# Optimization experiments

Measured on AMD Instinct MI355X. Metric: run time of the kernel, lower is better.

The kernel has to match this reference:

```python
import jax, jax.numpy as jnp
import numpy as np

B, S, D, H, V, L, N, FF = 4, 2048, 768, 4, 32000, 2048, 3, 1024
DH = D // H  # 192; note original scales scores by 1/20, not 1/sqrt(192)


def layernorm(x, g, b):
    m = jnp.mean(x, axis=-1, keepdims=True)
    v = jnp.mean((x - m) ** 2, axis=-1, keepdims=True)
    return (x - m) / jnp.sqrt(v + 1e-5) * g + b


def attn_block(h, Wq, bq, Wk, bk, Wv, bv, g, b, mask):
    Bx, Sx, _ = h.shape
    q = (h @ Wq + bq).reshape(Bx, Sx, H, DH).transpose(0, 2, 1, 3)  # bhsd
    k = (h @ Wk + bk).reshape(Bx, Sx, H, DH).transpose(0, 2, 1, 3)
    v = (h @ Wv + bv).reshape(Bx, Sx, H, DH).transpose(0, 2, 1, 3)
    w = jnp.einsum('bhqd,bhkd->bhqk', q, k) / 20.0
    w = jnp.where(mask, -1e9, w)
    # original code uses Softmax(dim=2), i.e. over the QUERY axis — kept faithful
    a = jax.nn.softmax(w, axis=2)
    o = jnp.einsum('bhqk,bhkd->bhqd', a, v)
    o = o.transpose(0, 2, 1, 3).reshape(Bx, Sx, D)
    return layernorm(h + o, g, b)


def setup_inputs() -> dict:
    key = jax.random.key(0)
    ks = jax.random.split(key, 12)
    sc = 0.02
    n = lambda k, s: jax.random.normal(k, s, jnp.float32) * sc
    return {
        'x': jax.random.randint(ks[0], (B, S), 0, V),
        'label': jax.random.randint(ks[1], (B, S), 0, V),
        'tok_emb': n(ks[2], (V, D)),
        'pos_emb': n(ks[3], (L, D)),
        'Wq': n(ks[4], (N, 2, D, D)), 'bq': jnp.zeros((N, 2, D)),
        'Wk': n(ks[5], (N, 2, D, D)), 'bk': jnp.zeros((N, 2, D)),
        'Wv': n(ks[6], (N, 2, D, D)), 'bv': jnp.zeros((N, 2, D)),
        'ln_g': jnp.ones((N, 2, D)), 'ln_b': jnp.zeros((N, 2, D)),
        'W1': n(ks[7], (N, D, FF)), 'b1': jnp.zeros((N, FF)),
        'W2': n(ks[8], (N, FF, D)), 'b2': jnp.zeros((N, D)),
        'f_g': jnp.ones((N, D)), 'f_b': jnp.zeros((N, D)),
        'Wcls': n(ks[9], (D, V)), 'bcls': jnp.zeros((V,)),
    }


def reference(x, label, tok_emb, pos_emb, Wq, bq, Wk, bk, Wv, bv, ln_g, ln_b,
              W1, b1, W2, b2, f_g, f_b, Wcls, bcls):
    Bx, Sx = x.shape
    pad = (x == 0)[:, None, :, None]                       # [B,1,S,1] masks query rows
    look = jnp.triu(jnp.ones((Sx, Sx), bool), 1)[None, None]
    mask = look | pad                                      # [B,1,S,S] -> broadcast over H
    h = tok_emb[x] + pos_emb[jnp.arange(Sx)][None, :, :]
    for i in range(N):
        for j in range(2):
            h = attn_block(h, Wq[i, j], bq[i, j], Wk[i, j], bk[i, j],
                           Wv[i, j], bv[i, j], ln_g[i, j], ln_b[i, j], mask)
        h1 = jax.nn.relu(h @ W1[i] + b1[i]) @ W2[i] + b2[i]
        h = layernorm(h + h1, f_g[i], f_b[i])
    logits = h @ Wcls + bcls                               # [B,S,V]
    logp = jax.nn.log_softmax(logits, axis=-1)
    loss = -jnp.mean(jnp.take_along_axis(logp, label[..., None], axis=-1))
    return loss
```

## Files before the change

### kernel.cpp

```cpp
#include <hip/hip_runtime.h>
#include <hip/hip_bf16.h>

using u16 = unsigned short;
using u32 = unsigned int;
using bf16x8 = __attribute__((ext_vector_type(8))) short;
using f32x4  = __attribute__((ext_vector_type(4))) float;

namespace {
constexpr int BB   = 4;
constexpr int SEQ  = 2048;
constexpr int DIM  = 768;
constexpr int NH   = 4;
constexpr int DHD  = 192;
constexpr int VOC  = 32000;
constexpr int NLAY = 3;
constexpr int FFD  = 1024;
constexpr int ROWS = BB * SEQ;
constexpr int NT2  = VOC / 256;
constexpr int QKV = 3 * DIM;
constexpr int BH  = BB * NH;
}

__device__ __forceinline__ float b2f(u16 u) { return __uint_as_float(((u32)u) << 16); }
__device__ __forceinline__ u16 f2b(float f) {
    u32 x = __float_as_uint(f);
    return (u16)((x + 0x7fffu + ((x >> 16) & 1u)) >> 16);
}

__device__ __forceinline__ void gload16(const u16* g, u16* l) {
    __builtin_amdgcn_global_load_lds(
        (const __attribute__((address_space(1))) u32*)g,
        (__attribute__((address_space(3))) u32*)l, 16, 0, 0);
}

#define PHASE_END(N) do {                                        \
    __builtin_amdgcn_sched_barrier(0);                           \
    asm volatile("s_waitcnt vmcnt(" #N ")" ::: "memory");        \
    __builtin_amdgcn_s_barrier();                                \
    asm volatile("" ::: "memory");                               \
    __builtin_amdgcn_sched_barrier(0);                           \
} while (0)

__device__ __forceinline__ float block_sum256(float v, float* sb) {
    #pragma unroll
    for (int off = 32; off > 0; off >>= 1) v += __shfl_down(v, off, 64);
    int lane = threadIdx.x & 63, w = threadIdx.x >> 6;
    if (lane == 0) sb[w] = v;
    __syncthreads();
    float r = sb[0] + sb[1] + sb[2] + sb[3];
    __syncthreads();
    return r;
}

template<int MODE>
__global__ __launch_bounds__(512, 2)
void gemm256(const u16* __restrict__ A, long lda,
             const u16* __restrict__ Bt, long ldb,
             int M, int N, int K,
             const float* __restrict__ bias,
             float* __restrict__ Cf, u16* __restrict__ Cb, long ldc,
             int relu,
             int HH, long sAb, long sAh, long sBb, long sBh, long sCb, long sCh,
             const int* __restrict__ xtok, float* __restrict__ cpart,
             const int* __restrict__ label,
             float* __restrict__ partials, float* __restrict__ picked)
{
    __shared__ __align__(16) u16 sA[2][256 * 64];
    __shared__ __align__(16) u16 sB[2][256 * 64];

    int t = threadIdx.x, w = t >> 6, lane = t & 63;
    int wr = w >> 2, wcn = w & 3;
    int lr = lane & 15, lg = lane >> 4, rsw = lr & 7;

    int z = blockIdx.z;
    int bz = z / HH, hz = z % HH;
    const u16* Ab = A + (size_t)bz * sAb + (size_t)hz * sAh;
    const u16* Bb = Bt + (size_t)bz * sBb + (size_t)hz * sBh;
    size_t Coff = (size_t)bz * sCb + (size_t)hz * sCh;

    int bx = blockIdx.x, by = blockIdx.y;
    if (MODE == 1) {
        int tix = blockIdx.x;
        by = 7;
        while (by * (by + 1) / 2 > tix) by--;
        bx = tix - by * (by + 1) / 2;
    } else {
        int pid = by * gridDim.x + bx;
        int xcd = pid & 7, s = pid >> 3;
        bx = s >> 2;
        by = xcd * 4 + (s & 3);
    }
    int m0 = by * 256, n0 = bx * 256;

    int srow = lane >> 3;
    int scol = ((lane & 7) ^ srow) * 8;

    f32x4 acc[8][4];
    #pragma unroll
    for (int i = 0; i < 8; i++)
        #pragma unroll
        for (int j = 0; j < 4; j++) acc[i][j] = (f32x4){0.f, 0.f, 0.f, 0.f};

    auto stageA = [&](int buf, int k0) {
        #pragma unroll
        for (int r = 0; r < 4; r++) {
            int rb = r * 64 + w * 8;
            gload16(Ab + (size_t)(m0 + rb + srow) * lda + k0 + scol,
                    &sA[buf][rb * 64]);
        }
    };
    auto stageB = [&](int buf, int k0, int h) {
        #pragma unroll
        for (int j = 0; j < 2; j++) {
            int rb = (j * 2 + (w >> 2)) * 64 + h * 32 + (w & 3) * 8;
            gload16(Bb + (size_t)(n0 + rb + srow) * ldb + k0 + scol,
                    &sB[buf][rb * 64]);
        }
    };

    {
        int nt = K >> 6;
        stageA(0, 0); stageB(0, 0, 0); stageB(0, 0, 1);
        PHASE_END(0);

        for (int kt = 0; kt < nt; ++kt) {
            int cur = kt & 1;
            int kn = (kt + 1) << 6;
            bool st = (kt + 1 < nt);
            bf16x8 aa[2][8], bb[2][2];
            #pragma unroll
            for (int kx = 0; kx < 2; kx++) {
                int jsw = ((kx * 4 + lg) ^ rsw) * 8;
                #pragma unroll
                for (int mi = 0; mi < 8; mi++)
                    aa[kx][mi] = *(const bf16x8*)&sA[cur][(wr * 128 + mi * 16 + lr) * 64 + jsw];
                #pragma unroll
                for (int ni = 0; ni < 2; ni++)
                    bb[kx][ni] = *(const bf16x8*)&sB[cur][(wcn * 64 + ni * 16 + lr) * 64 + jsw];
            }
            if (st) { stageA(cur ^ 1, kn); stageB(cur ^ 1, kn, 0); }
            __builtin_amdgcn_s_setprio(1);
            #pragma unroll
            for (int kx = 0; kx < 2; kx++)
                #pragma unroll
                for (int mi = 0; mi < 8; mi++)
                    #pragma unroll
                    for (int ni = 0; ni < 2; ni++)
                        acc[mi][ni] = __builtin_amdgcn_mfma_f32_16x16x32_bf16(
                            aa[kx][mi], bb[kx][ni], acc[mi][ni], 0, 0, 0);
            __builtin_amdgcn_s_setprio(0);
            if (st) PHASE_END(6); else PHASE_END(0);
            bf16x8 bc[2][2];
            #pragma unroll
            for (int kx = 0; kx < 2; kx++) {
                int jsw = ((kx * 4 + lg) ^ rsw) * 8;
                #pragma unroll
                for (int ni = 0; ni < 2; ni++)
                    bc[kx][ni] = *(const bf16x8*)&sB[cur][(wcn * 64 + (ni + 2) * 16 + lr) * 64 + jsw];
            }
            if (st) stageB(cur ^ 1, kn, 1);
            __builtin_amdgcn_s_setprio(1);
            #pragma unroll
            for (int kx = 0; kx < 2; kx++)
                #pragma unroll
                for (int mi = 0; mi < 8; mi++)
                    #pragma unroll
                    for (int ni = 0; ni < 2; ni++)
                        acc[mi][ni + 2] = __builtin_amdgcn_mfma_f32_16x16x32_bf16(
                            aa[kx][mi], bc[kx][ni], acc[mi][ni + 2], 0, 0, 0);
            __builtin_amdgcn_s_setprio(0);
            if (st) PHASE_END(2); else PHASE_END(0);
        }
    }

    if (MODE == 1) {
        const int* xb = xtok + (size_t)bz * SEQ;
        float cs[2][4] = {{0.f,0.f,0.f,0.f},{0.f,0.f,0.f,0.f}};
        #pragma unroll
        for (int mi = 0; mi < 8; mi++)
            #pragma unroll
            for (int j = 0; j < 4; j++) {
                int grow = m0 + wr * 128 + mi * 16 + lg * 4 + j;
                int xz = xb[grow];
                #pragma unroll
                for (int ni = 0; ni < 4; ni++) {
                    int gcol = n0 + wcn * 64 + ni * 16 + lr;
                    float v = acc[mi][ni][j] * 0.05f;
                    if (gcol > grow || xz == 0) v = -30.f;
                    float e = __expf(v);
                    Cb[Coff + (size_t)grow * ldc + gcol] = f2b(e);
                    cs[mi >> 2][ni] += e;
                }
            }
        #pragma unroll
        for (int h = 0; h < 2; h++)
            #pragma unroll
            for (int ni = 0; ni < 4; ni++) {
                float c = cs[h][ni];
                c += __shfl_xor(c, 16, 64);
                c += __shfl_xor(c, 32, 64);
                if (lg == 0) {
                    int p = (m0 >> 6) + wr * 2 + h;
                    cpart[((size_t)p * BH + z) * SEQ + n0 + wcn * 64 + ni * 16 + lr] = c;
                }
            }
    } else {
        #pragma unroll
        for (int mi = 0; mi < 8; mi++)
            #pragma unroll
            for (int ni = 0; ni < 4; ni++) {
                int gcol = n0 + wcn * 64 + ni * 16 + lr;
                float bcol = bias[gcol];
                #pragma unroll
                for (int j = 0; j < 4; j++) acc[mi][ni][j] += bcol;
            }
        #pragma unroll
        for (int mi = 0; mi < 8; mi++)
            #pragma unroll
            for (int j = 0; j < 4; j++) {
                int grow = m0 + wr * 128 + mi * 16 + lg * 4 + j;
                int lab = label[grow];
                #pragma unroll
                for (int ni = 0; ni < 4; ni++) {
                    int gcol = n0 + wcn * 64 + ni * 16 + lr;
                    if (lab == gcol) picked[grow] = acc[mi][ni][j];
                }
            }
        float* red = (float*)sA;
        #pragma unroll
        for (int mi = 0; mi < 8; mi++)
            #pragma unroll
            for (int j = 0; j < 4; j++) {
                float mx = -1e30f;
                #pragma unroll
                for (int ni = 0; ni < 4; ni++) mx = fmaxf(mx, acc[mi][ni][j]);
                #pragma unroll
                for (int off = 1; off < 16; off <<= 1)
                    mx = fmaxf(mx, __shfl_xor(mx, off, 64));
                float ss = 0.f;
                #pragma unroll
                for (int ni = 0; ni < 4; ni++) ss += __expf(acc[mi][ni][j] - mx);
                #pragma unroll
                for (int off = 1; off < 16; off <<= 1) ss += __shfl_xor(ss, off, 64);
                if (lr == 0) {
                    int rloc = wr * 128 + mi * 16 + lg * 4 + j;
                    red[rloc * 8 + wcn * 2 + 0] = mx;
                    red[rloc * 8 + wcn * 2 + 1] = ss;
                }
            }
        __syncthreads();
        if (t < 256) {
            float Mv = -1e30f;
            #pragma unroll
            for (int q = 0; q < 4; q++) Mv = fmaxf(Mv, red[t * 8 + q * 2]);
            float Sv = 0.f;
            #pragma unroll
            for (int q = 0; q < 4; q++)
                Sv += red[t * 8 + q * 2 + 1] * __expf(red[t * 8 + q * 2] - Mv);
            size_t row = (size_t)(m0 + t);
            partials[(row * NT2 + bx) * 2 + 0] = Mv;
            partials[(row * NT2 + bx) * 2 + 1] = Sv;
        }
    }
}

template<int MODE>
__global__ __launch_bounds__(256)
void gemm128(const u16* __restrict__ A, long lda,
             const u16* __restrict__ Bt, long ldb,
             int N, int K,
             const float* __restrict__ bias,
             float* __restrict__ Cf, u16* __restrict__ Cb, long ldc, int relu,
             int HH, long sAb, long sAh, long sBb, long sBh, long sCb, long sCh)
{
    __shared__ __align__(16) u16 sA[2][128 * 64];
    __shared__ __align__(16) u16 sB[2][128 * 64];

    int z = blockIdx.z, bz = z / HH, hz = z % HH;
    const u16* Ab = A + (size_t)bz * sAb + (size_t)hz * sAh;
    const u16* Bb = Bt + (size_t)bz * sBb + (size_t)hz * sBh;
    size_t Coff = (size_t)bz * sCb + (size_t)hz * sCh;

    int bx = blockIdx.x, by = blockIdx.y;
    if (MODE == 0 && gridDim.y == 64) {
        int pid = by * gridDim.x + bx;
        int xcd = pid & 7, s = pid >> 3;
        bx = s >> 3;
        by = xcd * 8 + (s & 7);
    }
    if (MODE == 3) {
        by = (by & 1) ? (15 - (by >> 1)) : (by >> 1);
    }
    int m0 = by * 128, n0 = bx * 128;

    int t = threadIdx.x, w = t >> 6, lane = t & 63;
    int wr = w >> 1, wc = w & 1, lr = lane & 15, lg = lane >> 4, rsw = lr & 7;
    int srow = lane >> 3, scol = ((lane & 7) ^ srow) * 8;

    f32x4 acc[4][4];
    #pragma unroll
    for (int i = 0; i < 4; i++)
        #pragma unroll
        for (int j = 0; j < 4; j++) acc[i][j] = (f32x4){0.f, 0.f, 0.f, 0.f};

    auto stageA = [&](int buf, int k0) {
        #pragma unroll
        for (int i = 0; i < 4; i++) {
            int rb = (w * 4 + i) * 8;
            gload16(Ab + (size_t)(m0 + rb + srow) * lda + k0 + scol,
                    &sA[buf][rb * 64]);
        }
    };
    auto stageB = [&](int buf, int k0, int h) {
        #pragma unroll
        for (int j = 0; j < 2; j++) {
            int rb = j * 64 + h * 32 + w * 8;
            int row = n0 + rb + srow;
            if (MODE == 3) { if (row > N - 1) row = N - 1; }
            gload16(Bb + (size_t)row * ldb + k0 + scol, &sB[buf][rb * 64]);
        }
    };

    int nt = K >> 6;
    if (MODE == 3) {
        int ntE = (by + 1) * 2;
        if (ntE < nt) nt = ntE;
    }

    stageA(0, 0); stageB(0, 0, 0); stageB(0, 0, 1);
    PHASE_END(0);

    for (int kt = 0; kt < nt; ++kt) {
        int cur = kt & 1;
        int kn = (kt + 1) << 6;
        bool st = (kt + 1 < nt);
        bf16x8 aa[2][4], bb[2][2];
        #pragma unroll
        for (int kx = 0; kx < 2; kx++) {
            int jsw = ((kx * 4 + lg) ^ rsw) * 8;
            #pragma unroll
            for (int mi = 0; mi < 4; mi++)
                aa[kx][mi] = *(const bf16x8*)&sA[cur][(wr * 64 + mi * 16 + lr) * 64 + jsw];
            #pragma unroll
            for (int ni = 0; ni < 2; ni++)
                bb[kx][ni] = *(const bf16x8*)&sB[cur][(wc * 64 + ni * 16 + lr) * 64 + jsw];
        }
        if (st) { stageA(cur ^ 1, kn); stageB(cur ^ 1, kn, 0); }
        __builtin_amdgcn_s_setprio(1);
        #pragma unroll
        for (int kx = 0; kx < 2; kx++)
            #pragma unroll
            for (int mi = 0; mi < 4; mi++)
                #pragma unroll
                for (int ni = 0; ni < 2; ni++)
                    acc[mi][ni] = __builtin_amdgcn_mfma_f32_16x16x32_bf16(
                        aa[kx][mi], bb[kx][ni], acc[mi][ni], 0, 0, 0);
        __builtin_amdgcn_s_setprio(0);
        if (st) PHASE_END(6); else PHASE_END(0);

        bf16x8 bc[2][2];
        #pragma unroll
        for (int kx = 0; kx < 2; kx++) {
            int jsw = ((kx * 4 + lg) ^ rsw) * 8;
            #pragma unroll
            for (int ni = 0; ni < 2; ni++)
                bc[kx][ni] = *(const bf16x8*)&sB[cur][(wc * 64 + (ni + 2) * 16 + lr) * 64 + jsw];
        }
        if (st) stageB(cur ^ 1, kn, 1);
        __builtin_amdgcn_s_setprio(1);
        #pragma unroll
        for (int kx = 0; kx < 2; kx++)
            #pragma unroll
            for (int mi = 0; mi < 4; mi++)
                #pragma unroll
                for (int ni = 0; ni < 2; ni++)
                    acc[mi][ni + 2] = __builtin_amdgcn_mfma_f32_16x16x32_bf16(
                        aa[kx][mi], bc[kx][ni], acc[mi][ni + 2], 0, 0, 0);
        __builtin_amdgcn_s_setprio(0);
        if (st) PHASE_END(2); else PHASE_END(0);
    }

    #pragma unroll
    for (int mi = 0; mi < 4; mi++)
        #pragma unroll
        for (int ni = 0; ni < 4; ni++)
            #pragma unroll
            for (int j = 0; j < 4; j++) {
                int grow = m0 + wr * 64 + mi * 16 + lg * 4 + j;
                int gcol = n0 + wc * 64 + ni * 16 + lr;
                if (MODE == 3) {
                    if (gcol < N)
                        Cb[Coff + (size_t)grow * ldc + gcol] = f2b(acc[mi][ni][j]);
                } else {
                    float v = acc[mi][ni][j];
                    if (bias) v += bias[gcol];
                    if (relu) v = fmaxf(v, 0.f);
                    size_t ci = Coff + (size_t)grow * ldc + gcol;
                    if (Cf) Cf[ci] = v;
                    if (Cb) Cb[ci] = f2b(v);
                }
            }
}

__global__ __launch_bounds__(256)
void embed_k(const int* __restrict__ x, const float* __restrict__ tok,
             const float* __restrict__ pos, u16* __restrict__ hb)
{
    int row = blockIdx.x, t = threadIdx.x;
    int token = x[row];
    int s = row & (SEQ - 1);
    size_t base = (size_t)row * DIM;
    #pragma unroll
    for (int e = 0; e < 3; e++) {
        int d = t + e * 256;
        float v = tok[(size_t)token * DIM + d] + pos[(size_t)s * DIM + d];
        hb[base + d] = f2b(v);
    }
}

__global__ __launch_bounds__(256)
void resid_ln(const u16* __restrict__ res, const u16* __restrict__ add,
              const float* __restrict__ g, const float* __restrict__ b,
              u16* __restrict__ out)
{
    __shared__ float sb[4];
    int row = blockIdx.x, t = threadIdx.x;
    size_t base = (size_t)row * DIM;
    float x0 = 0.f, x1 = 0.f, x2 = 0.f, x3 = 0.f;
    if (t < 192) {
        ushort4 r4 = *(const ushort4*)&res[base + t * 4];
        ushort4 a4 = *(const ushort4*)&add[base + t * 4];
        x0 = b2f(r4.x) + b2f(a4.x);
        x1 = b2f(r4.y) + b2f(a4.y);
        x2 = b2f(r4.z) + b2f(a4.z);
        x3 = b2f(r4.w) + b2f(a4.w);
    }
    float mean = block_sum256(x0 + x1 + x2 + x3, sb) * (1.f / DIM);
    float d0 = x0 - mean, d1 = x1 - mean, d2 = x2 - mean, d3 = x3 - mean;
    float var = block_sum256(t < 192 ? d0*d0 + d1*d1 + d2*d2 + d3*d3 : 0.f, sb) * (1.f / DIM);
    float rs = rsqrtf(var + 1e-5f);
    if (t < 192) {
        float4 gv = *(const float4*)&g[t * 4];
        float4 bv = *(const float4*)&b[t * 4];
        ushort4 ob = {f2b(d0 * rs * gv.x + bv.x), f2b(d1 * rs * gv.y + bv.y),
                      f2b(d2 * rs * gv.z + bv.z), f2b(d3 * rs * gv.w + bv.w)};
        *(ushort4*)&out[base + t * 4] = ob;
    }
}

__global__ void v_transpose(const u16* __restrict__ v, long ldv,
                            const float* __restrict__ cpart, u16* __restrict__ vT)
{
    __shared__ u16 tile[32][33];
    int z = blockIdx.z;
    int b = z >> 2, h = z & 3;
    int s0 = blockIdx.x * 32, d0 = blockIdx.y * 32;
    int tx = threadIdx.x, ty = threadIdx.y;
    #pragma unroll
    for (int i = 0; i < 4; i++)
        tile[ty + i * 8][tx] = v[((size_t)b * SEQ + s0 + ty + i * 8) * ldv + h * DHD + d0 + tx];
    int scol = s0 + tx;
    int pmin = (scol >> 8) * 4;
    float sv = 0.f;
    for (int p = pmin; p < 32; p++) sv += cpart[((size_t)p * BH + z) * SEQ + scol];
    float inv = 1.f / sv;
    __syncthreads();
    #pragma unroll
    for (int i = 0; i < 4; i++)
        vT[((size_t)z * DHD + d0 + ty + i * 8) * SEQ + scol] =
            f2b(b2f(tile[tx][ty + i * 8]) * inv);
}

__global__ void wt_cvt(const float* __restrict__ src, u16* __restrict__ dst, int K, int N)
{
    __shared__ float tile[32][33];
    int n0 = blockIdx.x * 32, k0 = blockIdx.y * 32;
    int tx = threadIdx.x, ty = threadIdx.y;
    #pragma unroll
    for (int i = 0; i < 4; i++)
        tile[ty + i * 8][tx] = src[(size_t)(k0 + ty + i * 8) * N + n0 + tx];
    __syncthreads();
    #pragma unroll
    for (int i = 0; i < 4; i++)
        dst[(size_t)(n0 + ty + i * 8) * K + k0 + tx] = f2b(tile[tx][ty + i * 8]);
}

__global__ __launch_bounds__(256)
void bias_cat(const float* __restrict__ bq, const float* __restrict__ bk,
              const float* __restrict__ bv, float* __restrict__ dst)
{
    int ij = blockIdx.x, t = threadIdx.x;
    #pragma unroll
    for (int e = 0; e < 3; e++) {
        int d = t + e * 256;
        dst[(size_t)ij * QKV + d]            = bq[(size_t)ij * DIM + d];
        dst[(size_t)ij * QKV + DIM + d]      = bk[(size_t)ij * DIM + d];
        dst[(size_t)ij * QKV + 2 * DIM + d]  = bv[(size_t)ij * DIM + d];
    }
}

__global__ __launch_bounds__(256)
void lse_merge(const float* __restrict__ partials, float* __restrict__ lse)
{
    __shared__ float sm[4], ssum[4];
    int row = blockIdx.x, t = threadIdx.x;
    float m = -1e30f, s = 0.f;
    if (t < NT2) {
        const float* p = partials + ((size_t)row * NT2 + t) * 2;
        m = p[0]; s = p[1];
    }
    #pragma unroll
    for (int off = 1; off < 64; off <<= 1) {
        float om = __shfl_xor(m, off, 64), os = __shfl_xor(s, off, 64);
        float M = fmaxf(m, om);
        s = s * __expf(m - M) + os * __expf(om - M);
        m = M;
    }
    int lane = t & 63, w = t >> 6;
    if (lane == 0) { sm[w] = m; ssum[w] = s; }
    __syncthreads();
    if (t == 0) {
        float M = fmaxf(fmaxf(sm[0], sm[1]), fmaxf(sm[2], sm[3]));
        float S = ssum[0] * __expf(sm[0] - M) + ssum[1] * __expf(sm[1] - M) +
                  ssum[2] * __expf(sm[2] - M) + ssum[3] * __expf(sm[3] - M);
        lse[row] = M + __logf(S);
    }
}

__global__ __launch_bounds__(256)
void loss_k(const float* __restrict__ lse, const float* __restrict__ picked,
            float* __restrict__ out)
{
    __shared__ float sb[4];
    int t = threadIdx.x;
    float a = 0.f;
    for (int r = t; r < ROWS; r += 256) a += lse[r] - picked[r];
    float tot = block_sum256(a, sb);
    if (t == 0) out[0] = tot / (float)ROWS;
}

extern "C" void kernel_launch(void* const* d_in, const int* in_sizes, int n_in,
                              void* d_out, int out_size, void* d_ws, size_t ws_size,
                              hipStream_t stream)
{
    (void)in_sizes; (void)n_in; (void)out_size; (void)ws_size;
    const int*   x     = (const int*)d_in[0];
    const int*   label = (const int*)d_in[1];
    const float* tok   = (const float*)d_in[2];
    const float* pos   = (const float*)d_in[3];
    const float* Wq    = (const float*)d_in[4];
    const float* bq    = (const float*)d_in[5];
    const float* Wk    = (const float*)d_in[6];
    const float* bk    = (const float*)d_in[7];
    const float* Wv    = (const float*)d_in[8];
    const float* bv    = (const float*)d_in[9];
    const float* ln_g  = (const float*)d_in[10];
    const float* ln_b  = (const float*)d_in[11];
    const float* W1    = (const float*)d_in[12];
    const float* b1    = (const float*)d_in[13];
    const float* W2    = (const float*)d_in[14];
    const float* b2    = (const float*)d_in[15];
    const float* f_g   = (const float*)d_in[16];
    const float* f_b   = (const float*)d_in[17];
    const float* Wcls  = (const float*)d_in[18];
    const float* bcls  = (const float*)d_in[19];

    char* p = (char*)d_ws;
    auto alloc = [&](size_t bytes) -> char* {
        char* r = p;
        p += (bytes + 255) & ~(size_t)255;
        return r;
    };
    u16* hb     = (u16*)alloc((size_t)ROWS * DIM * 2);
    u16* ob     = (u16*)alloc((size_t)ROWS * DIM * 2);
    u16* qkvb   = (u16*)alloc((size_t)ROWS * QKV * 2);
    u16* vTb    = (u16*)alloc((size_t)BH * DHD * SEQ * 2);
    u16* ff1b   = (u16*)alloc((size_t)ROWS * FFD * 2);
    u16* wbuf   = (u16*)alloc((size_t)BH * SEQ * SEQ * 2);
    u16* WqkvT  = (u16*)alloc((size_t)6 * QKV * DIM * 2);
    u16* W1T    = (u16*)alloc((size_t)NLAY * DIM * FFD * 2);
    u16* W2T    = (u16*)alloc((size_t)NLAY * FFD * DIM * 2);
    u16* WcT    = (u16*)alloc((size_t)DIM * VOC * 2);
    float* bqkv = (float*)alloc((size_t)6 * QKV * 4);
    float* cpart= (float*)alloc((size_t)32 * BH * SEQ * 4);
    float* partials = (float*)alloc((size_t)ROWS * NT2 * 2 * 4);
    float* picked   = (float*)alloc((size_t)ROWS * 4);
    float* lsev     = (float*)alloc((size_t)ROWS * 4);

    dim3 t32(32, 8, 1);
    for (int ij = 0; ij < 6; ij++) {
        wt_cvt<<<dim3(DIM / 32, DIM / 32, 1), t32, 0, stream>>>(
            Wq + (size_t)ij * DIM * DIM, WqkvT + (size_t)ij * QKV * DIM, DIM, DIM);
        wt_cvt<<<dim3(DIM / 32, DIM / 32, 1), t32, 0, stream>>>(
            Wk + (size_t)ij * DIM * DIM, WqkvT + (size_t)ij * QKV * DIM + (size_t)DIM * DIM, DIM, DIM);
        wt_cvt<<<dim3(DIM / 32, DIM / 32, 1), t32, 0, stream>>>(
            Wv + (size_t)ij * DIM * DIM, WqkvT + (size_t)ij * QKV * DIM + (size_t)2 * DIM * DIM, DIM, DIM);
    }
    bias_cat<<<6, 256, 0, stream>>>(bq, bk, bv, bqkv);
    for (int i = 0; i < NLAY; i++) {
        wt_cvt<<<dim3(FFD / 32, DIM / 32, 1), t32, 0, stream>>>(
            W1 + (size_t)i * DIM * FFD, W1T + (size_t)i * DIM * FFD, DIM, FFD);
        wt_cvt<<<dim3(DIM / 32, FFD / 32, 1), t32, 0, stream>>>(
            W2 + (size_t)i * FFD * DIM, W2T + (size_t)i * FFD * DIM, FFD, DIM);
    }
    wt_cvt<<<dim3(VOC / 32, DIM / 32, 1), t32, 0, stream>>>(Wcls, WcT, DIM, VOC);

    embed_k<<<ROWS, 256, 0, stream>>>(x, tok, pos, hb);

    for (int i = 0; i < NLAY; i++) {
        for (int j = 0; j < 2; j++) {
            int ij = i * 2 + j;
            gemm128<0><<<dim3(QKV / 128, ROWS / 128, 1), 256, 0, stream>>>(
                hb, DIM, WqkvT + (size_t)ij * QKV * DIM, DIM, QKV, DIM,
                bqkv + (size_t)ij * QKV, nullptr, qkvb, QKV, 0,
                1, 0, 0, 0, 0, 0, 0);
            gemm256<1><<<dim3(36, 1, BH), 512, 0, stream>>>(
                qkvb, QKV, qkvb + DIM, QKV, SEQ, SEQ, DHD,
                nullptr, nullptr, wbuf, SEQ, 0,
                NH, (long)SEQ * QKV, (long)DHD, (long)SEQ * QKV, (long)DHD,
                (long)NH * SEQ * SEQ, (long)SEQ * SEQ,
                x, cpart, nullptr, nullptr, nullptr);
            v_transpose<<<dim3(SEQ / 32, DHD / 32, BH), t32, 0, stream>>>(
                qkvb + 2 * DIM, QKV, cpart, vTb);
            gemm128<3><<<dim3(2, SEQ / 128, BH), 256, 0, stream>>>(
                wbuf, SEQ, vTb, SEQ, DHD, SEQ,
                nullptr, nullptr, ob, DIM, 0,
                NH, (long)NH * SEQ * SEQ, (long)SEQ * SEQ,
                (long)NH * DHD * SEQ, (long)DHD * SEQ,
                (long)SEQ * DIM, (long)DHD);
            resid_ln<<<ROWS, 256, 0, stream>>>(
                hb, ob, ln_g + (size_t)ij * DIM, ln_b + (size_t)ij * DIM, hb);
        }
        gemm128<0><<<dim3(FFD / 128, ROWS / 128, 1), 256, 0, stream>>>(
            hb, DIM, W1T + (size_t)i * DIM * FFD, DIM, FFD, DIM,
            b1 + (size_t)i * FFD, nullptr, ff1b, FFD, 1,
            1, 0, 0, 0, 0, 0, 0);
        gemm128<0><<<dim3(DIM / 128, ROWS / 128, 1), 256, 0, stream>>>(
            ff1b, FFD, W2T + (size_t)i * FFD * DIM, FFD, DIM, FFD,
            b2 + (size_t)i * DIM, nullptr, ob, DIM, 0,
            1, 0, 0, 0, 0, 0, 0);
        resid_ln<<<ROWS, 256, 0, stream>>>(
            hb, ob, f_g + (size_t)i * DIM, f_b + (size_t)i * DIM, hb);
    }

    gemm256<2><<<dim3(NT2, ROWS / 256, 1), 512, 0, stream>>>(
        hb, DIM, WcT, DIM, ROWS, VOC, DIM,
        bcls, nullptr, nullptr, 0, 0,
        1, 0, 0, 0, 0, 0, 0,
        nullptr, nullptr, label, partials, picked);
    lse_merge<<<ROWS, 256, 0, stream>>>(partials, lsev);
    loss_k<<<1, 256, 0, stream>>>(lsev, picked, (float*)d_out);
}
```

Baseline: 2.153 ms.

## Run classifier GEMM in FP8 e4m3 with fused log-softmax epilogue

Adds an FP8 (e4m3) path for the vocab-projection GEMM. The hidden state is quantized with a fixed x4 scale and the classifier weights with a fixed x16 scale, and MFMA fp8 instructions are used with 128-wide K tiles. The goal is to halve operand bandwidth and LDS traffic and to use the higher-throughput fp8 MFMA for the largest GEMM. The cost is an extra quantization kernel and precision loss on the logits, which relies on fixed static scales that suit the weight and activation magnitudes. The old gemm256 MODE 2 path and the unused float-output arguments are removed.

Result: faster. 2.083 ms (-3.3%).

```diff
diff --git a/kernel.cpp b/kernel.cpp
--- a/kernel.cpp
+++ b/kernel.cpp
@@ -3,6 +3,8 @@
 
 using u16 = unsigned short;
 using u32 = unsigned int;
+using u8  = unsigned char;
+using u64 = unsigned long long;
 using bf16x8 = __attribute__((ext_vector_type(8))) short;
 using f32x4  = __attribute__((ext_vector_type(4))) float;
 
@@ -27,7 +29,23 @@
     return (u16)((x + 0x7fffu + ((x >> 16) & 1u)) >> 16);
 }
 
+__device__ __forceinline__ u32 f2e4m3(float f) {
+    float af = fabsf(f);
+    u32 sgn = (__float_as_uint(f) >> 24) & 0x80u;
+    if (!(af < 448.f)) return sgn | 0x7Eu;
+    int e = (int)((__float_as_uint(af) >> 23) & 0xff) - 127;
+    if (e < -6) e = -6;
+    float sc = __uint_as_float((u32)(130 - e) << 23);
+    int code = __float2int_rn(af * sc) + ((e + 6) << 3);
+    return sgn | (u32)code;
+}
+
 __device__ __forceinline__ void gload16(const u16* g, u16* l) {
+    __builtin_amdgcn_global_load_lds(
+        (const __attribute__((address_space(1))) u32*)g,
+        (__attribute__((address_space(3))) u32*)l, 16, 0, 0);
+}
+__device__ __forceinline__ void gload16b(const u8* g, u8* l) {
     __builtin_amdgcn_global_load_lds(
         (const __attribute__((address_space(1))) u32*)g,
         (__attribute__((address_space(3))) u32*)l, 16, 0, 0);
@@ -57,13 +75,9 @@
 void gemm256(const u16* __restrict__ A, long lda,
              const u16* __restrict__ Bt, long ldb,
              int M, int N, int K,
-             const float* __restrict__ bias,
-             float* __restrict__ Cf, u16* __restrict__ Cb, long ldc,
-             int relu,
+             u16* __restrict__ Cb, long ldc,
              int HH, long sAb, long sAh, long sBb, long sBh, long sCb, long sCh,
-             const int* __restrict__ xtok, float* __restrict__ cpart,
-             const int* __restrict__ label,
-             float* __restrict__ partials, float* __restrict__ picked)
+             const int* __restrict__ xtok, float* __restrict__ cpart)
 {
     __shared__ __align__(16) u16 sA[2][256 * 64];
     __shared__ __align__(16) u16 sB[2][256 * 64];
@@ -79,16 +93,11 @@
     size_t Coff = (size_t)bz * sCb + (size_t)hz * sCh;
 
     int bx = blockIdx.x, by = blockIdx.y;
-    if (MODE == 1) {
+    {
         int tix = blockIdx.x;
         by = 7;
         while (by * (by + 1) / 2 > tix) by--;
         bx = tix - by * (by + 1) / 2;
-    } else {
-        int pid = by * gridDim.x + bx;
-        int xcd = pid & 7, s = pid >> 3;
-        bx = s >> 2;
-        by = xcd * 4 + (s & 3);
     }
     int m0 = by * 256, n0 = bx * 256;
 
@@ -150,6 +159,7 @@
                             aa[kx][mi], bb[kx][ni], acc[mi][ni], 0, 0, 0);
             __builtin_amdgcn_s_setprio(0);
             if (st) PHASE_END(6); else PHASE_END(0);
+
             bf16x8 bc[2][2];
             #pragma unroll
             for (int kx = 0; kx < 2; kx++) {
@@ -173,7 +183,7 @@
         }
     }
 
-    if (MODE == 1) {
+    {
         const int* xb = xtok + (size_t)bz * SEQ;
         float cs[2][4] = {{0.f,0.f,0.f,0.f},{0.f,0.f,0.f,0.f}};
         #pragma unroll
@@ -204,63 +214,168 @@
                     cpart[((size_t)p * BH + z) * SEQ + n0 + wcn * 64 + ni * 16 + lr] = c;
                 }
             }
-    } else {
-        #pragma unroll
-        for (int mi = 0; mi < 8; mi++)
+    }
+}
+
+__global__ __launch_bounds__(512, 2)
+void gemm256_f8(const u8* __restrict__ Aq, const u8* __restrict__ Bq, int K,
+                const float* __restrict__ bias,
+                const int* __restrict__ label,
+                float* __restrict__ partials, float* __restrict__ picked)
+{
+    __shared__ __align__(16) u8 sA8[2][256 * 128];
+    __shared__ __align__(16) u8 sB8[2][2][128 * 128];
+
+    int t = threadIdx.x, w = t >> 6, lane = t & 63;
+    int wr = w >> 2, wcn = w & 3;
+    int lr = lane & 15, lg = lane >> 4;
+    int swz = (lr & 7) * 16;
+
+    int bx = blockIdx.x, by = blockIdx.y;
+    {
+        int pid = by * gridDim.x + bx;
+        int xcd = pid & 7, s = pid >> 3;
+        bx = s >> 2;
+        by = xcd * 4 + (s & 3);
+    }
+    int m0 = by * 256, n0 = bx * 256;
+
+    int srow8 = lane >> 3;
+    int scol8 = ((lane & 7) ^ srow8) * 16;
+
+    f32x4 acc[8][4];
+    #pragma unroll
+    for (int i = 0; i < 8; i++)
+        #pragma unroll
+        for (int j = 0; j < 4; j++) acc[i][j] = (f32x4){0.f, 0.f, 0.f, 0.f};
+
+    auto stageA = [&](int buf, int k0) {
+        #pragma unroll
+        for (int i = 0; i < 4; i++) {
+            int rb = i * 64 + w * 8;
+            gload16b(Aq + (size_t)(m0 + rb + srow8) * DIM + k0 + scol8,
+                     &sA8[buf][rb * 128]);
+        }
+    };
+    auto stageB = [&](int buf, int k0, int h) {
+        #pragma unroll
+        for (int j = 0; j < 2; j++) {
+            int rh = j * 64 + w * 8;
+            int rbase = (rh >> 5) * 64 + h * 32 + (rh & 31);
+            gload16b(Bq + (size_t)(n0 + rbase + srow8) * DIM + k0 + scol8,
+                     &sB8[buf][h][rh * 128]);
+        }
+    };
+
+    int nt = K >> 7;
+    stageA(0, 0); stageB(0, 0, 0); stageB(0, 0, 1);
+    PHASE_END(0);
+
+    for (int kt = 0; kt < nt; ++kt) {
+        int cur = kt & 1;
+        int kn = (kt + 1) << 7;
+        bool st = (kt + 1 < nt);
+        long aa[4][8], bb[4][2];
+        #pragma unroll
+        for (int s = 0; s < 4; s++) {
+            int off = (s * 32 + lg * 8) ^ swz;
+            #pragma unroll
+            for (int mi = 0; mi < 8; mi++)
+                aa[s][mi] = *(const long*)&sA8[cur][(wr * 128 + mi * 16 + lr) * 128 + off];
+            #pragma unroll
+            for (int ni = 0; ni < 2; ni++)
+                bb[s][ni] = *(const long*)&sB8[cur][0][(wcn * 32 + ni * 16 + lr) * 128 + off];
+        }
+        if (st) { stageA(cur ^ 1, kn); stageB(cur ^ 1, kn, 0); }
+        __builtin_amdgcn_s_setprio(1);
+        #pragma unroll
+        for (int s = 0; s < 4; s++)
+            #pragma unroll
+            for (int mi = 0; mi < 8; mi++)
+                #pragma unroll
+                for (int ni = 0; ni < 2; ni++)
+                    acc[mi][ni] = __builtin_amdgcn_mfma_f32_16x16x32_fp8_fp8(
+                        aa[s][mi], bb[s][ni], acc[mi][ni], 0, 0, 0);
+        __builtin_amdgcn_s_setprio(0);
+        if (st) PHASE_END(6); else PHASE_END(0);
+        long bc[4][2];
+        #pragma unroll
+        for (int s = 0; s < 4; s++) {
+            int off = (s * 32 + lg * 8) ^ swz;
+            #pragma unroll
+            for (int ni = 0; ni < 2; ni++)
+                bc[s][ni] = *(const long*)&sB8[cur][1][(wcn * 32 + ni * 16 + lr) * 128 + off];
+        }
+        if (st) stageB(cur ^ 1, kn, 1);
+        __builtin_amdgcn_s_setprio(1);
+        #pragma unroll
+        for (int s = 0; s < 4; s++)
+            #pragma unroll
+            for (int mi = 0; mi < 8; mi++)
+                #pragma unroll
+                for (int ni = 0; ni < 2; ni++)
+                    acc[mi][ni + 2] = __builtin_amdgcn_mfma_f32_16x16x32_fp8_fp8(
+                        aa[s][mi], bc[s][ni], acc[mi][ni + 2], 0, 0, 0);
+        __builtin_amdgcn_s_setprio(0);
+        if (st) PHASE_END(2); else PHASE_END(0);
+    }
+
+    #pragma unroll
+    for (int mi = 0; mi < 8; mi++)
+        #pragma unroll
+        for (int ni = 0; ni < 4; ni++) {
+            int gcol = n0 + wcn * 64 + ni * 16 + lr;
+            float bcol = bias[gcol];
+            #pragma unroll
+            for (int j = 0; j < 4; j++)
+                acc[mi][ni][j] = acc[mi][ni][j] * (1.f / 64.f) + bcol;
+        }
+    #pragma unroll
+    for (int mi = 0; mi < 8; mi++)
+        #pragma unroll
+        for (int j = 0; j < 4; j++) {
+            int grow = m0 + wr * 128 + mi * 16 + lg * 4 + j;
+            int lab = label[grow];
             #pragma unroll
             for (int ni = 0; ni < 4; ni++) {
                 int gcol = n0 + wcn * 64 + ni * 16 + lr;
-                float bcol = bias[gcol];
-                #pragma unroll
-                for (int j = 0; j < 4; j++) acc[mi][ni][j] += bcol;
+                if (lab == gcol) picked[grow] = acc[mi][ni][j];
             }
-        #pragma unroll
-        for (int mi = 0; mi < 8; mi++)
-            #pragma unroll
-            for (int j = 0; j < 4; j++) {
-                int grow = m0 + wr * 128 + mi * 16 + lg * 4 + j;
-                int lab = label[grow];
-                #pragma unroll
-                for (int ni = 0; ni < 4; ni++) {
-                    int gcol = n0 + wcn * 64 + ni * 16 + lr;
-                    if (lab == gcol) picked[grow] = acc[mi][ni][j];
-                }
+        }
+    float* red = (float*)sA8;
+    #pragma unroll
+    for (int mi = 0; mi < 8; mi++)
+        #pragma unroll
+        for (int j = 0; j < 4; j++) {
+            float mx = -1e30f;
+            #pragma unroll
+            for (int ni = 0; ni < 4; ni++) mx = fmaxf(mx, acc[mi][ni][j]);
+            #pragma unroll
+            for (int off = 1; off < 16; off <<= 1)
+                mx = fmaxf(mx, __shfl_xor(mx, off, 64));
+            float ss = 0.f;
+            #pragma unroll
+            for (int ni = 0; ni < 4; ni++) ss += __expf(acc[mi][ni][j] - mx);
+            #pragma unroll
+            for (int off = 1; off < 16; off <<= 1) ss += __shfl_xor(ss, off, 64);
+            if (lr == 0) {
+                int rloc = wr * 128 + mi * 16 + lg * 4 + j;
+                red[rloc * 8 + wcn * 2 + 0] = mx;
+                red[rloc * 8 + wcn * 2 + 1] = ss;
             }
-        float* red = (float*)sA;
-        #pragma unroll
-        for (int mi = 0; mi < 8; mi++)
-            #pragma unroll
-            for (int j = 0; j < 4; j++) {
-                float mx = -1e30f;
-                #pragma unroll
-                for (int ni = 0; ni < 4; ni++) mx = fmaxf(mx, acc[mi][ni][j]);
-                #pragma unroll
-                for (int off = 1; off < 16; off <<= 1)
-                    mx = fmaxf(mx, __shfl_xor(mx, off, 64));
-                float ss = 0.f;
-                #pragma unroll
-                for (int ni = 0; ni < 4; ni++) ss += __expf(acc[mi][ni][j] - mx);
-                #pragma unroll
-                for (int off = 1; off < 16; off <<= 1) ss += __shfl_xor(ss, off, 64);
-                if (lr == 0) {
-                    int rloc = wr * 128 + mi * 16 + lg * 4 + j;
-                    red[rloc * 8 + wcn * 2 + 0] = mx;
-                    red[rloc * 8 + wcn * 2 + 1] = ss;
-                }
-            }
-        __syncthreads();
-        if (t < 256) {
-            float Mv = -1e30f;
-            #pragma unroll
-            for (int q = 0; q < 4; q++) Mv = fmaxf(Mv, red[t * 8 + q * 2]);
-            float Sv = 0.f;
-            #pragma unroll
-            for (int q = 0; q < 4; q++)
-                Sv += red[t * 8 + q * 2 + 1] * __expf(red[t * 8 + q * 2] - Mv);
-            size_t row = (size_t)(m0 + t);
-            partials[(row * NT2 + bx) * 2 + 0] = Mv;
-            partials[(row * NT2 + bx) * 2 + 1] = Sv;
-        }
+        }
+    __syncthreads();
+    if (t < 256) {
+        float Mv = -1e30f;
+        #pragma unroll
+        for (int q = 0; q < 4; q++) Mv = fmaxf(Mv, red[t * 8 + q * 2]);
+        float Sv = 0.f;
+        #pragma unroll
+        for (int q = 0; q < 4; q++)
+            Sv += red[t * 8 + q * 2 + 1] * __expf(red[t * 8 + q * 2] - Mv);
+        size_t row = (size_t)(m0 + t);
+        partials[(row * NT2 + bx) * 2 + 0] = Mv;
+        partials[(row * NT2 + bx) * 2 + 1] = Sv;
     }
 }
 
@@ -270,7 +385,7 @@
              const u16* __restrict__ Bt, long ldb,
              int N, int K,
              const float* __restrict__ bias,
-             float* __restrict__ Cf, u16* __restrict__ Cb, long ldc, int relu,
+             u16* __restrict__ Cb, long ldc, int relu,
              int HH, long sAb, long sAh, long sBb, long sBh, long sCb, long sCh)
 {
     __shared__ __align__(16) u16 sA[2][128 * 64];
@@ -395,9 +510,7 @@
                     float v = acc[mi][ni][j];
                     if (bias) v += bias[gcol];
                     if (relu) v = fmaxf(v, 0.f);
-                    size_t ci = Coff + (size_t)grow * ldc + gcol;
-                    if (Cf) Cf[ci] = v;
-                    if (Cb) Cb[ci] = f2b(v);
+                    Cb[Coff + (size_t)grow * ldc + gcol] = f2b(v);
                 }
             }
 }
@@ -448,6 +561,18 @@
     }
 }
 
+__global__ __launch_bounds__(256)
+void h_to_fp8(const u16* __restrict__ hb, u8* __restrict__ hq)
+{
+    size_t idx = (size_t)blockIdx.x * 256 + threadIdx.x;
+    bf16x8 v = *(const bf16x8*)&hb[idx * 8];
+    u64 o = 0;
+    #pragma unroll
+    for (int e = 0; e < 8; e++)
+        o |= (u64)f2e4m3(b2f((u16)v[e]) * 4.f) << (8 * e);
+    *(u64*)&hq[idx * 8] = o;
+}
+
 __global__ void v_transpose(const u16* __restrict__ v, long ldv,
                             const float* __restrict__ cpart, u16* __restrict__ vT)
 {
@@ -483,6 +608,21 @@
     #pragma unroll
     for (int i = 0; i < 4; i++)
         dst[(size_t)(n0 + ty + i * 8) * K + k0 + tx] = f2b(tile[tx][ty + i * 8]);
+}
+
+__global__ void wt_cvt8(const float* __restrict__ src, u8* __restrict__ dst, int K, int N)
+{
+    __shared__ float tile[32][33];
+    int n0 = blockIdx.x * 32, k0 = blockIdx.y * 32;
+    int tx = threadIdx.x, ty = threadIdx.y;
+    #pragma unroll
+    for (int i = 0; i < 4; i++)
+        tile[ty + i * 8][tx] = src[(size_t)(k0 + ty + i * 8) * N + n0 + tx];
+    __syncthreads();
+    #pragma unroll
+    for (int i = 0; i < 4; i++)
+        dst[(size_t)(n0 + ty + i * 8) * K + k0 + tx] =
+            (u8)f2e4m3(tile[tx][ty + i * 8] * 16.f);
 }
 
 __global__ __launch_bounds__(256)
@@ -580,7 +720,8 @@
     u16* WqkvT  = (u16*)alloc((size_t)6 * QKV * DIM * 2);
     u16* W1T    = (u16*)alloc((size_t)NLAY * DIM * FFD * 2);
     u16* W2T    = (u16*)alloc((size_t)NLAY * FFD * DIM * 2);
-    u16* WcT    = (u16*)alloc((size_t)DIM * VOC * 2);
+    u8*  WcT8   = (u8*)alloc((size_t)DIM * VOC);
+    u8*  hq     = (u8*)alloc((size_t)ROWS * DIM);
     float* bqkv = (float*)alloc((size_t)6 * QKV * 4);
     float* cpart= (float*)alloc((size_t)32 * BH * SEQ * 4);
     float* partials = (float*)alloc((size_t)ROWS * NT2 * 2 * 4);
@@ -603,7 +744,7 @@
         wt_cvt<<<dim3(DIM / 32, FFD / 32, 1), t32, 0, stream>>>(
             W2 + (size_t)i * FFD * DIM, W2T + (size_t)i * FFD * DIM, FFD, DIM);
     }
-    wt_cvt<<<dim3(VOC / 32, DIM / 32, 1), t32, 0, stream>>>(Wcls, WcT, DIM, VOC);
+    wt_cvt8<<<dim3(VOC / 32, DIM / 32, 1), t32, 0, stream>>>(Wcls, WcT8, DIM, VOC);
 
     embed_k<<<ROWS, 256, 0, stream>>>(x, tok, pos, hb);
 
@@ -612,19 +753,19 @@
             int ij = i * 2 + j;
             gemm128<0><<<dim3(QKV / 128, ROWS / 128, 1), 256, 0, stream>>>(
                 hb, DIM, WqkvT + (size_t)ij * QKV * DIM, DIM, QKV, DIM,
-                bqkv + (size_t)ij * QKV, nullptr, qkvb, QKV, 0,
+                bqkv + (size_t)ij * QKV, qkvb, QKV, 0,
                 1, 0, 0, 0, 0, 0, 0);
             gemm256<1><<<dim3(36, 1, BH), 512, 0, stream>>>(
                 qkvb, QKV, qkvb + DIM, QKV, SEQ, SEQ, DHD,
-                nullptr, nullptr, wbuf, SEQ, 0,
+                wbuf, SEQ,
                 NH, (long)SEQ * QKV, (long)DHD, (long)SEQ * QKV, (long)DHD,
                 (long)NH * SEQ * SEQ, (long)SEQ * SEQ,
-                x, cpart, nullptr, nullptr, nullptr);
+                x, cpart);
             v_transpose<<<dim3(SEQ / 32, DHD / 32, BH), t32, 0, stream>>>(
                 qkvb + 2 * DIM, QKV, cpart, vTb);
             gemm128<3><<<dim3(2, SEQ / 128, BH), 256, 0, stream>>>(
                 wbuf, SEQ, vTb, SEQ, DHD, SEQ,
-                nullptr, nullptr, ob, DIM, 0,
+                nullptr, ob, DIM, 0,
                 NH, (long)NH * SEQ * SEQ, (long)SEQ * SEQ,
                 (long)NH * DHD * SEQ, (long)DHD * SEQ,
                 (long)SEQ * DIM, (long)DHD);
@@ -633,21 +774,19 @@
         }
         gemm128<0><<<dim3(FFD / 128, ROWS / 128, 1), 256, 0, stream>>>(
             hb, DIM, W1T + (size_t)i * DIM * FFD, DIM, FFD, DIM,
-            b1 + (size_t)i * FFD, nullptr, ff1b, FFD, 1,
+            b1 + (size_t)i * FFD, ff1b, FFD, 1,
             1, 0, 0, 0, 0, 0, 0);
         gemm128<0><<<dim3(DIM / 128, ROWS / 128, 1), 256, 0, stream>>>(
             ff1b, FFD, W2T + (size_t)i * FFD * DIM, FFD, DIM, FFD,
-            b2 + (size_t)i * DIM, nullptr, ob, DIM, 0,
+            b2 + (size_t)i * DIM, ob, DIM, 0,
             1, 0, 0, 0, 0, 0, 0);
         resid_ln<<<ROWS, 256, 0, stream>>>(
             hb, ob, f_g + (size_t)i * DIM, f_b + (size_t)i * DIM, hb);
     }
 
-    gemm256<2><<<dim3(NT2, ROWS / 256, 1), 512, 0, stream>>>(
-        hb, DIM, WcT, DIM, ROWS, VOC, DIM,
-        bcls, nullptr, nullptr, 0, 0,
-        1, 0, 0, 0, 0, 0, 0,
-        nullptr, nullptr, label, partials, picked);
+    h_to_fp8<<<(ROWS * DIM / 8) / 256, 256, 0, stream>>>(hb, hq);
+    gemm256_f8<<<dim3(NT2, ROWS / 256, 1), 512, 0, stream>>>(
+        hq, WcT8, DIM, bcls, label, partials, picked);
     lse_merge<<<ROWS, 256, 0, stream>>>(partials, lsev);
     loss_k<<<1, 256, 0, stream>>>(lsev, picked, (float*)d_out);
 }
```
